# Optimization experiments

Measured on AMD Instinct MI355X. Metric: run time of the kernel, lower is better.

Reference implementation:

```python
import jax, jax.numpy as jnp
import numpy as np

C = 128          # channels
L = 2            # num_layers
NA = 30000       # nodes of type 'a'
NB = 30000       # nodes of type 'b'
E = 150000       # edges per edge type
SEED_SIZE = 1024
EPS = 1e-5


def _ln(x, g, b):
    # LayerNorm over last dim (biased variance, eps=1e-5), matches nn.LayerNorm / PyG LayerNorm(mode='node')
    m = x.mean(-1, keepdims=True)
    v = ((x - m) ** 2).mean(-1, keepdims=True)
    return (x - m) * jax.lax.rsqrt(v + EPS) * g + b


def _seg_mean(msg, dst, n):
    # PyG aggr='mean': mean of incoming messages, 0 for isolated nodes
    s = jax.ops.segment_sum(msg, dst, num_segments=n)
    cnt = jax.ops.segment_sum(jnp.ones((dst.shape[0],), msg.dtype), dst, num_segments=n)
    return s / jnp.maximum(cnt, 1.0)[:, None]


def _prmp_conv(x_src, x_dst, edge, w1, b1, w2, b2, g, be, uw, ub):
    src, dst = edge[0], edge[1]
    xi = x_dst[dst]                                   # [E, C] dst feats per edge
    xj = x_src[src]                                   # [E, C] src feats per edge
    h = jax.nn.relu(jax.lax.stop_gradient(xi) @ w1 + b1)  # pred_mlp on detached x_i
    pred = h @ w2 + b2
    msg = _ln(xj - pred, g, be)                       # LayerNorm(residual) per edge
    agg = _seg_mean(msg, dst, x_dst.shape[0])         # mean aggregation to dst nodes
    return jax.nn.relu(jnp.concatenate([x_dst, agg], -1) @ uw + ub)  # update_mlp


def setup_inputs() -> dict:
    key = jax.random.key(0)
    ks = jax.random.split(key, 12)
    edge_ab = jnp.stack([jax.random.randint(ks[2], (E,), 0, NA, jnp.int32),
                         jax.random.randint(ks[3], (E,), 0, NB, jnp.int32)])
    edge_ba = jnp.stack([jax.random.randint(ks[4], (E,), 0, NB, jnp.int32),
                         jax.random.randint(ks[5], (E,), 0, NA, jnp.int32)])
    return {
        "x_a": jax.random.normal(ks[0], (NA, C), jnp.float32),
        "x_b": jax.random.normal(ks[1], (NB, C), jnp.float32),
        "edge_ab": edge_ab,
        "edge_ba": edge_ba,
        "pred_w1": jax.random.normal(ks[6], (L, 2, C, C), jnp.float32) * 0.05,
        "pred_b1": jnp.zeros((L, 2, C), jnp.float32),
        "pred_w2": jax.random.normal(ks[7], (L, 2, C, C), jnp.float32) * 0.05,
        "pred_b2": jnp.zeros((L, 2, C), jnp.float32),
        "msg_gamma": jnp.ones((L, 2, C), jnp.float32),
        "msg_beta": jnp.zeros((L, 2, C), jnp.float32),
        "upd_w": jax.random.normal(ks[8], (L, 2, 2 * C, C), jnp.float32) * 0.05,
        "upd_b": jnp.zeros((L, 2, C), jnp.float32),
        "node_gamma": jnp.ones((L, 2, C), jnp.float32),
        "node_beta": jnp.zeros((L, 2, C), jnp.float32),
        "head_w": jax.random.normal(ks[9], (C, 1), jnp.float32) * 0.05,
        "head_b": jnp.zeros((1,), jnp.float32),
        "seed_size": SEED_SIZE,
    }


def reference(x_a, x_b, edge_ab, edge_ba, pred_w1, pred_b1, pred_w2, pred_b2,
              msg_gamma, msg_beta, upd_w, upd_b, node_gamma, node_beta,
              head_w, head_b, seed_size):
    enc = lambda t: jnp.nan_to_num(t, nan=0.0, posinf=1.0, neginf=-1.0)
    x_a, x_b = enc(x_a), enc(x_b)
    for l in range(L):
        # edge type 0: a -> b ; edge type 1: b -> a (HeteroConv aggr='sum' is trivial: one conv per dst type)
        nb = _prmp_conv(x_a, x_b, edge_ab, pred_w1[l, 0], pred_b1[l, 0], pred_w2[l, 0], pred_b2[l, 0],
                        msg_gamma[l, 0], msg_beta[l, 0], upd_w[l, 0], upd_b[l, 0])
        na = _prmp_conv(x_b, x_a, edge_ba, pred_w1[l, 1], pred_b1[l, 1], pred_w2[l, 1], pred_b2[l, 1],
                        msg_gamma[l, 1], msg_beta[l, 1], upd_w[l, 1], upd_b[l, 1])
        na = jnp.nan_to_num(na, nan=0.0, posinf=10.0, neginf=-10.0)
        nb = jnp.nan_to_num(nb, nan=0.0, posinf=10.0, neginf=-10.0)
        x_a = jax.nn.relu(_ln(na, node_gamma[l, 0], node_beta[l, 0]))
        x_b = jax.nn.relu(_ln(nb, node_gamma[l, 1], node_beta[l, 1]))
    # head: single Linear(C -> 1) on the seed nodes of the entity table (type 'a')
    return x_a[:seed_size] @ head_w + head_b
```

## Files before the change

kernel.cpp:

```cpp
#include <hip/hip_runtime.h>

#define CC 128
#define SCAN_T 1024
#define SCAN_I 4

typedef __attribute__((ext_vector_type(8))) short bf16x8;
typedef __attribute__((ext_vector_type(4))) float f32x4;
#define MFMA16(a, b, c) __builtin_amdgcn_mfma_f32_16x16x32_bf16(a, b, c, 0, 0, 0)

__device__ __forceinline__ float enc_nan(float v) {
    if (v != v) return 0.f;
    if (v > 3.0e38f) return 1.f;
    if (v < -3.0e38f) return -1.f;
    return v;
}

__device__ __forceinline__ ushort f2bf(float x) {
    unsigned u = __builtin_bit_cast(unsigned, x);
    u += 0x7fff + ((u >> 16) & 1);
    return (ushort)(u >> 16);
}
__device__ __forceinline__ float bf2f(ushort h) {
    return __builtin_bit_cast(float, ((unsigned)h) << 16);
}

__device__ __forceinline__ int swz128(int row, int k) { return (row * 128 + k) ^ ((row & 7) << 3); }

__global__ __launch_bounds__(256)
void k_setup(const float* __restrict__ xa_in, ushort* __restrict__ xa,
             float2* __restrict__ stat_a, int NA,
             const float* __restrict__ xb_in, ushort* __restrict__ xb,
             float2* __restrict__ stat_b, int NB,
             const float* __restrict__ pw1, const float* __restrict__ pw2,
             const float* __restrict__ uw,
             ushort* __restrict__ w1t, ushort* __restrict__ w2t, ushort* __restrict__ uwt,
             const int* __restrict__ dst_b, int Eab, int* __restrict__ cnt_b,
             const int* __restrict__ dst_a, int Eba, int* __restrict__ cnt_a,
             int Ginit, int Gwcvt)
{
    const int b = blockIdx.x;
    const int tid = threadIdx.x;
    if (b < Ginit) {
        int row = b * 8 + (tid >> 5);
        int s = tid & 31;
        const float* xin; ushort* xo; float2* st;
        if (row < NA) { xin = xa_in; xo = xa; st = stat_a; }
        else {
            row -= NA;
            if (row >= NB) return;
            xin = xb_in; xo = xb; st = stat_b;
        }
        float4 v = *reinterpret_cast<const float4*>(xin + (size_t)row * CC + s * 4);
        ushort h0 = f2bf(enc_nan(v.x)), h1 = f2bf(enc_nan(v.y));
        ushort h2 = f2bf(enc_nan(v.z)), h3 = f2bf(enc_nan(v.w));
        *reinterpret_cast<ushort4*>(xo + (size_t)row * CC + s * 4) = make_ushort4(h0, h1, h2, h3);
        float r0 = bf2f(h0), r1 = bf2f(h1), r2 = bf2f(h2), r3 = bf2f(h3);
        float sm = (r0 + r1) + (r2 + r3);
        float sq = fmaf(r0, r0, fmaf(r1, r1, fmaf(r2, r2, r3 * r3)));
        #pragma unroll
        for (int m = 1; m < 32; m <<= 1) { sm += __shfl_xor(sm, m); sq += __shfl_xor(sq, m); }
        if (s == 0) st[row] = make_float2(sm, sq);
    } else if (b < Ginit + Gwcvt) {
        int i = (b - Ginit) * 256 + tid;
        int t = i >> 16;
        int r = i & 65535;
        if (r < 16384) {
            int k = r >> 7, c = r & 127;
            w1t[(size_t)t * 16384 + c * 128 + k] = f2bf(pw1[(size_t)t * 16384 + k * 128 + c]);
        } else if (r < 32768) {
            int rr = r - 16384;
            int k = rr >> 7, c = rr & 127;
            w2t[(size_t)t * 16384 + c * 128 + k] = f2bf(pw2[(size_t)t * 16384 + k * 128 + c]);
        } else {
            int rr = r - 32768;
            int k = rr >> 7, c = rr & 127;
            uwt[(size_t)t * 32768 + c * 256 + k] = f2bf(uw[(size_t)t * 32768 + k * 128 + c]);
        }
    } else {
        int i = (b - Ginit - Gwcvt) * 256 + tid;
        if (i < Eab) atomicAdd(&cnt_b[dst_b[i]], 1);
        else if (i - Eab < Eba) atomicAdd(&cnt_a[dst_a[i - Eab]], 1);
    }
}

__global__ __launch_bounds__(SCAN_T)
void k_scan_dual(const int* __restrict__ cnt0, int* __restrict__ rowp0, int* __restrict__ off0, int n0,
                 const int* __restrict__ cnt1, int* __restrict__ rowp1, int* __restrict__ off1, int n1)
{
    const int* cnt = (blockIdx.x == 0) ? cnt0 : cnt1;
    int* row_ptr   = (blockIdx.x == 0) ? rowp0 : rowp1;
    int* off       = (blockIdx.x == 0) ? off0 : off1;
    int n          = (blockIdx.x == 0) ? n0 : n1;

    __shared__ int wsum[SCAN_T / 64];
    __shared__ int carry_s;
    const int tid = threadIdx.x, lane = tid & 63, wid = tid >> 6;
    if (tid == 0) carry_s = 0;
    __syncthreads();
    const int chunk = SCAN_T * SCAN_I;
    for (int base = 0; base < n; base += chunk) {
        int i0 = base + tid * SCAN_I;
        int v[SCAN_I];
        int local = 0;
        #pragma unroll
        for (int t = 0; t < SCAN_I; ++t) {
            int i = i0 + t;
            v[t] = (i < n) ? cnt[i] : 0;
            local += v[t];
        }
        int incl = local;
        #pragma unroll
        for (int d = 1; d < 64; d <<= 1) {
            int t = __shfl_up(incl, d);
            if (lane >= d) incl += t;
        }
        if (lane == 63) wsum[wid] = incl;
        __syncthreads();
        if (wid == 0) {
            int wv = (lane < SCAN_T / 64) ? wsum[lane] : 0;
            int winc = wv;
            #pragma unroll
            for (int d = 1; d < SCAN_T / 64; d <<= 1) {
                int t = __shfl_up(winc, d);
                if (lane >= d) winc += t;
            }
            if (lane < SCAN_T / 64) wsum[lane] = winc - wv;
        }
        __syncthreads();
        int carry = carry_s;
        int excl = carry + wsum[wid] + incl - local;
        #pragma unroll
        for (int t = 0; t < SCAN_I; ++t) {
            int i = i0 + t;
            if (i < n) { row_ptr[i] = excl; off[i] = excl; }
            excl += v[t];
        }
        __syncthreads();
        if (tid == SCAN_T - 1) carry_s = carry + wsum[SCAN_T / 64 - 1] + incl;
        __syncthreads();
    }
    if (threadIdx.x == 0) row_ptr[n] = carry_s;
}

__global__ __launch_bounds__(256)
void k_scatter_dual(const int* __restrict__ src_b, const int* __restrict__ dst_b, int Eab,
                    int* __restrict__ off_b, int* __restrict__ srcs_ab,
                    const int* __restrict__ src_a, const int* __restrict__ dst_a, int Eba,
                    int* __restrict__ off_a, int* __restrict__ srcs_ba)
{
    int i = blockIdx.x * 256 + threadIdx.x;
    if (i < Eab) {
        int p = atomicAdd(&off_b[dst_b[i]], 1);
        srcs_ab[p] = src_b[i];
    } else if (i - Eab < Eba) {
        int j = i - Eab;
        int p = atomicAdd(&off_a[dst_a[j]], 1);
        srcs_ba[p] = src_a[j];
    }
}

__device__ __forceinline__ void layer_body(
    char* smem,
    const ushort* __restrict__ xdst, const ushort* __restrict__ xsrc,
    const float2* __restrict__ stat_src,
    const int* __restrict__ rowp, const int* __restrict__ srcs,
    const ushort* __restrict__ w1t, const float* __restrict__ b1,
    const ushort* __restrict__ w2t, const float* __restrict__ b2,
    const float* __restrict__ mg, const float* __restrict__ mbt,
    const ushort* __restrict__ uwt, const float* __restrict__ ub,
    const float* __restrict__ ng, const float* __restrict__ nb,
    ushort* __restrict__ xout, float2* __restrict__ statOut, int N, int blk,
    const float* __restrict__ hw, const float* __restrict__ hb,
    float* __restrict__ hout, int headS)
{
    ushort* As = (ushort*)smem;
    ushort* Hs = (ushort*)(smem + 8192);
    ushort* P  = (ushort*)(smem + 16384);
    float (*os)[CC + 4] = (float(*)[CC + 4])(smem + 8192);

    const int tid = threadIdx.x;
    const int base = blk * 32;
    const int w = tid >> 6, l = tid & 63;
    const int lr = l & 15, lg = l >> 4;
    const int quarter = l >> 4;
    const int c8 = (l & 15) * 8;

    const int n0 = base + w * 8;
    int rp[9];
    #pragma unroll
    for (int i = 0; i < 9; ++i) {
        int nn = n0 + i;
        rp[i] = rowp[nn < N ? nn : N];
    }

    {
        int row = tid >> 3, k0 = (tid & 7) << 4;
        int node = base + row;
        bf16x8 v0 = {}, v1 = {};
        if (node < N) {
            v0 = *reinterpret_cast<const bf16x8*>(xdst + (size_t)node * CC + k0);
            v1 = *reinterpret_cast<const bf16x8*>(xdst + (size_t)node * CC + k0 + 8);
        }
        *reinterpret_cast<bf16x8*>(&As[swz128(row, k0)])     = v0;
        *reinterpret_cast<bf16x8*>(&As[swz128(row, k0 + 8)]) = v1;
    }
    __syncthreads();

    {
        f32x4 acc[2][2] = {};
        for (int kb = 0; kb < 4; ++kb) {
            int k = kb * 32 + lg * 8;
            bf16x8 a0 = *reinterpret_cast<const bf16x8*>(&As[swz128(lr, k)]);
            bf16x8 a1 = *reinterpret_cast<const bf16x8*>(&As[swz128(lr + 16, k)]);
            bf16x8 b0 = *reinterpret_cast<const bf16x8*>(&w1t[(size_t)(w * 32 + lr) * 128 + k]);
            bf16x8 b1v = *reinterpret_cast<const bf16x8*>(&w1t[(size_t)(w * 32 + 16 + lr) * 128 + k]);
            acc[0][0] = MFMA16(a0, b0, acc[0][0]);
            acc[0][1] = MFMA16(a0, b1v, acc[0][1]);
            acc[1][0] = MFMA16(a1, b0, acc[1][0]);
            acc[1][1] = MFMA16(a1, b1v, acc[1][1]);
        }
        float bc[2] = { b1[w * 32 + lr], b1[w * 32 + 16 + lr] };
        #pragma unroll
        for (int mi = 0; mi < 2; ++mi)
            #pragma unroll
            for (int ni = 0; ni < 2; ++ni) {
                int col = w * 32 + ni * 16 + lr;
                #pragma unroll
                for (int j = 0; j < 4; ++j) {
                    int row = mi * 16 + lg * 4 + j;
                    Hs[swz128(row, col)] = f2bf(fmaxf(acc[mi][ni][j] + bc[ni], 0.f));
                }
            }
    }
    __syncthreads();

    {
        f32x4 acc[2][2] = {};
        for (int kb = 0; kb < 4; ++kb) {
            int k = kb * 32 + lg * 8;
            bf16x8 a0 = *reinterpret_cast<const bf16x8*>(&Hs[swz128(lr, k)]);
            bf16x8 a1 = *reinterpret_cast<const bf16x8*>(&Hs[swz128(lr + 16, k)]);
            bf16x8 b0 = *reinterpret_cast<const bf16x8*>(&w2t[(size_t)(w * 32 + lr) * 128 + k]);
            bf16x8 b1v = *reinterpret_cast<const bf16x8*>(&w2t[(size_t)(w * 32 + 16 + lr) * 128 + k]);
            acc[0][0] = MFMA16(a0, b0, acc[0][0]);
            acc[0][1] = MFMA16(a0, b1v, acc[0][1]);
            acc[1][0] = MFMA16(a1, b0, acc[1][0]);
            acc[1][1] = MFMA16(a1, b1v, acc[1][1]);
        }
        float bc[2] = { b2[w * 32 + lr], b2[w * 32 + 16 + lr] };
        #pragma unroll
        for (int mi = 0; mi < 2; ++mi)
            #pragma unroll
            for (int ni = 0; ni < 2; ++ni) {
                int col = w * 32 + ni * 16 + lr;
                #pragma unroll
                for (int j = 0; j < 4; ++j) {
                    int row = mi * 16 + lg * 4 + j;
                    P[row * CC + col] = f2bf(acc[mi][ni][j] + bc[ni]);
                }
            }
    }
    __syncthreads();

    {
        const float4 g0 = *reinterpret_cast<const float4*>(mg + c8);
        const float4 g1 = *reinterpret_cast<const float4*>(mg + c8 + 4);
        const float4 e0 = *reinterpret_cast<const float4*>(mbt + c8);
        const float4 e1 = *reinterpret_cast<const float4*>(mbt + c8 + 4);
        const float gv[8] = { g0.x, g0.y, g0.z, g0.w, g1.x, g1.y, g1.z, g1.w };
        const float bv[8] = { e0.x, e0.y, e0.z, e0.w, e1.x, e1.y, e1.z, e1.w };

        int pj = rp[0] + quarter;
        bool phave = pj < rp[1];
        int psidx = srcs[phave ? pj : 0];
        bf16x8 pxv = *reinterpret_cast<const bf16x8*>(xsrc + (size_t)psidx * CC + c8);
        float2 pst = stat_src[psidx];

        for (int i = 0; i < 8; ++i) {
            const int nl_ = w * 8 + i;
            const int d = n0 + i;
            bool chave = phave;
            bf16x8 cxv = pxv;
            float2 cst = pst;
            int cj = rp[i] + quarter;
            const int je = rp[i + 1];
            if (i < 7) {
                pj = rp[i + 1] + quarter;
                phave = pj < rp[i + 2];
                psidx = srcs[phave ? pj : 0];
                pxv = *reinterpret_cast<const bf16x8*>(xsrc + (size_t)psidx * CC + c8);
                pst = stat_src[psidx];
            }
            if (d >= N) continue;

            bf16x8 prb = *reinterpret_cast<const bf16x8*>(&P[nl_ * CC + c8]);
            float pr[8];
            #pragma unroll
            for (int q = 0; q < 8; ++q) pr[q] = bf2f((ushort)prb[q]);
            float sp = 0.f, qp = 0.f;
            #pragma unroll
            for (int q = 0; q < 8; ++q) { sp += pr[q]; qp = fmaf(pr[q], pr[q], qp); }
            #pragma unroll
            for (int m = 1; m < 16; m <<= 1) { sp += __shfl_xor(sp, m); qp += __shfl_xor(qp, m); }
            const int deg = je - rp[i];
            float a[8] = {};
            float rsum = 0.f, cmsum = 0.f;

            while (chave) {
                int jn = cj + 4;
                bool nhave = jn < je;
                bf16x8 nxv = cxv; float2 nst = cst;
                if (nhave) {
                    int nsidx = srcs[jn];
                    nxv = *reinterpret_cast<const bf16x8*>(xsrc + (size_t)nsidx * CC + c8);
                    nst = stat_src[nsidx];
                }
                float xj[8];
                #pragma unroll
                for (int q = 0; q < 8; ++q) xj[q] = bf2f((ushort)cxv[q]);
                float dot = 0.f;
                #pragma unroll
                for (int q = 0; q < 8; ++q) dot = fmaf(xj[q], pr[q], dot);
                #pragma unroll
                for (int m = 1; m < 16; m <<= 1) dot += __shfl_xor(dot, m);
                const float mean = (cst.x - sp) * (1.f / 128.f);
                const float var = fmaf(-2.f, dot, cst.y + qp) * (1.f / 128.f) - mean * mean;
                const float r = rsqrtf(var + 1e-5f);
                rsum += r;
                cmsum = fmaf(mean, r, cmsum);
                #pragma unroll
                for (int q = 0; q < 8; ++q) a[q] = fmaf(xj[q], r, a[q]);
                cj = jn; chave = nhave; cxv = nxv; cst = nst;
            }
            #pragma unroll
            for (int q = 0; q < 8; ++q) { a[q] += __shfl_xor(a[q], 16); a[q] += __shfl_xor(a[q], 32); }
            rsum += __shfl_xor(rsum, 16);  rsum += __shfl_xor(rsum, 32);
            cmsum += __shfl_xor(cmsum, 16); cmsum += __shfl_xor(cmsum, 32);
            if (quarter == 0) {
                ushort o8[8];
                if (deg > 0) {
                    const float inv = 1.f / (float)deg;
                    #pragma unroll
                    for (int q = 0; q < 8; ++q)
                        o8[q] = f2bf(fmaf((a[q] - pr[q] * rsum - cmsum) * inv, gv[q], bv[q]));
                } else {
                    #pragma unroll
                    for (int q = 0; q < 8; ++q) o8[q] = 0;
                }
                *reinterpret_cast<bf16x8*>(&Hs[swz128(nl_, c8)]) = *reinterpret_cast<bf16x8*>(&o8[0]);
            }
        }
    }
    __syncthreads();

    f32x4 acc[2][2] = {};
    for (int kb = 0; kb < 8; ++kb) {
        int k = kb * 32 + lg * 8;
        const ushort* Ab = (k < 128) ? As : Hs;
        int kl = k & 127;
        bf16x8 a0 = *reinterpret_cast<const bf16x8*>(&Ab[swz128(lr, kl)]);
        bf16x8 a1 = *reinterpret_cast<const bf16x8*>(&Ab[swz128(lr + 16, kl)]);
        bf16x8 b0 = *reinterpret_cast<const bf16x8*>(&uwt[(size_t)(w * 32 + lr) * 256 + k]);
        bf16x8 b1v = *reinterpret_cast<const bf16x8*>(&uwt[(size_t)(w * 32 + 16 + lr) * 256 + k]);
        acc[0][0] = MFMA16(a0, b0, acc[0][0]);
        acc[0][1] = MFMA16(a0, b1v, acc[0][1]);
        acc[1][0] = MFMA16(a1, b0, acc[1][0]);
        acc[1][1] = MFMA16(a1, b1v, acc[1][1]);
    }
    __syncthreads();

    {
        float bc[2] = { ub[w * 32 + lr], ub[w * 32 + 16 + lr] };
        #pragma unroll
        for (int mi = 0; mi < 2; ++mi)
            #pragma unroll
            for (int ni = 0; ni < 2; ++ni) {
                int col = w * 32 + ni * 16 + lr;
                #pragma unroll
                for (int j = 0; j < 4; ++j) {
                    int row = mi * 16 + lg * 4 + j;
                    os[row][col] = fmaxf(acc[mi][ni][j] + bc[ni], 0.f);
                }
            }
    }
    __syncthreads();

    const int nl = w * 8 + (l >> 3);
    const int cl = l & 7;
    float vals[16];
    float sm = 0.f, sq = 0.f;
    #pragma unroll
    for (int t = 0; t < 16; ++t) {
        float u = os[nl][cl + 8 * t];
        vals[t] = u; sm += u; sq = fmaf(u, u, sq);
    }
    #pragma unroll
    for (int m = 1; m < 8; m <<= 1) { sm += __shfl_xor(sm, m); sq += __shfl_xor(sq, m); }
    float mean = sm * (1.f / 128.f);
    float var = sq * (1.f / 128.f) - mean * mean;
    float r = rsqrtf(var + 1e-5f);
    int node = base + nl;
    if (node < N) {
        float so = 0.f, sqo = 0.f, hsum = 0.f;
        bool doHead = (node < headS);
        #pragma unroll
        for (int t = 0; t < 16; ++t) {
            int cch = cl + 8 * t;
            float o = fmaxf(fmaf((vals[t] - mean) * r, ng[cch], nb[cch]), 0.f);
            ushort ob = f2bf(o);
            xout[(size_t)node * CC + cch] = ob;
            float orr = bf2f(ob);
            so += orr; sqo = fmaf(orr, orr, sqo);
            if (doHead) hsum = fmaf(o, hw[cch], hsum);
        }
        #pragma unroll
        for (int m = 1; m < 8; m <<= 1) { so += __shfl_xor(so, m); sqo += __shfl_xor(sqo, m); }
        if (doHead) {
            #pragma unroll
            for (int m = 1; m < 8; m <<= 1) hsum += __shfl_xor(hsum, m);
            if (cl == 0) hout[node] = hsum + hb[0];
        }
        if (cl == 0) statOut[node] = make_float2(so, sqo);
    }
}

__global__ __launch_bounds__(256)
void k_layer_dual(
    const ushort* __restrict__ xb_c, const ushort* __restrict__ xa_c,
    const float2* __restrict__ stat_a_c, const float2* __restrict__ stat_b_c,
    const int* __restrict__ rowp_b, const int* __restrict__ srcs_ab,
    const int* __restrict__ rowp_a, const int* __restrict__ srcs_ba,
    ushort* __restrict__ xb_n, ushort* __restrict__ xa_n,
    float2* __restrict__ stat_b_n, float2* __restrict__ stat_a_n,
    int NB, int NA, int GB,
    const ushort* __restrict__ w1t0, const float* __restrict__ b10,
    const ushort* __restrict__ w2t0, const float* __restrict__ b20,
    const float* __restrict__ mg0, const float* __restrict__ mb0,
    const ushort* __restrict__ uwt0, const float* __restrict__ ub0,
    const float* __restrict__ ng0, const float* __restrict__ nb0,
    const ushort* __restrict__ w1t1, const float* __restrict__ b11,
    const ushort* __restrict__ w2t1, const float* __restrict__ b21,
    const float* __restrict__ mg1, const float* __restrict__ mb1,
    const ushort* __restrict__ uwt1, const float* __restrict__ ub1,
    const float* __restrict__ ng1, const float* __restrict__ nb1,
    const float* __restrict__ hw, const float* __restrict__ hb,
    float* __restrict__ hout, int headS)
{
    __shared__ __align__(16) char smem[25088];
    if ((int)blockIdx.x < GB)
        layer_body(smem, xb_c, xa_c, stat_a_c, rowp_b, srcs_ab,
                   w1t0, b10, w2t0, b20, mg0, mb0, uwt0, ub0, ng0, nb0,
                   xb_n, stat_b_n, NB, blockIdx.x, hw, hb, hout, 0);
    else
        layer_body(smem, xa_c, xb_c, stat_b_c, rowp_a, srcs_ba,
                   w1t1, b11, w2t1, b21, mg1, mb1, uwt1, ub1, ng1, nb1,
                   xa_n, stat_a_n, NA, blockIdx.x - GB, hw, hb, hout, headS);
}

extern "C" void kernel_launch(void* const* d_in, const int* in_sizes, int n_in,
                              void* d_out, int out_size, void* d_ws, size_t ws_size,
                              hipStream_t stream)
{
    const float* x_a_in = (const float*)d_in[0];
    const float* x_b_in = (const float*)d_in[1];
    const int*   e_ab   = (const int*)d_in[2];
    const int*   e_ba   = (const int*)d_in[3];
    const float* pw1    = (const float*)d_in[4];
    const float* pb1    = (const float*)d_in[5];
    const float* pw2    = (const float*)d_in[6];
    const float* pb2    = (const float*)d_in[7];
    const float* mgam   = (const float*)d_in[8];
    const float* mbet   = (const float*)d_in[9];
    const float* uw     = (const float*)d_in[10];
    const float* ubias  = (const float*)d_in[11];
    const float* ngam   = (const float*)d_in[12];
    const float* nbet   = (const float*)d_in[13];
    const float* hw     = (const float*)d_in[14];
    const float* hb     = (const float*)d_in[15];

    const int NA  = in_sizes[0] / CC;
    const int NB  = in_sizes[1] / CC;
    const int Eab = in_sizes[2] / 2;
    const int Eba = in_sizes[3] / 2;

    float* ws = (float*)d_ws;
    size_t off = 0;
    ushort* xa0 = (ushort*)(ws + off); off += (size_t)NA * CC / 2;
    ushort* xa1 = (ushort*)(ws + off); off += (size_t)NA * CC / 2;
    ushort* xb0 = (ushort*)(ws + off); off += (size_t)NB * CC / 2;
    ushort* xb1 = (ushort*)(ws + off); off += (size_t)NB * CC / 2;
    float2* sa0 = (float2*)(ws + off); off += (size_t)NA * 2;
    float2* sa1 = (float2*)(ws + off); off += (size_t)NA * 2;
    float2* sb0 = (float2*)(ws + off); off += (size_t)NB * 2;
    float2* sb1 = (float2*)(ws + off); off += (size_t)NB * 2;
    ushort* w1t = (ushort*)(ws + off); off += 4 * 16384 / 2;
    ushort* w2t = (ushort*)(ws + off); off += 4 * 16384 / 2;
    ushort* uwt = (ushort*)(ws + off); off += 4 * 32768 / 2;
    int* iw = (int*)(ws + off);
    size_t ioff = 0;
    int* cnt_b   = iw + ioff; ioff += NB;
    int* cnt_a   = iw + ioff; ioff += NA;
    int* rowp_b  = iw + ioff; ioff += NB + 1;
    int* rowp_a  = iw + ioff; ioff += NA + 1;
    int* off_b   = iw + ioff; ioff += NB;
    int* off_a   = iw + ioff; ioff += NA;
    int* srcs_ab = iw + ioff; ioff += Eab;
    int* srcs_ba = iw + ioff; ioff += Eba;

    const int GB = (NB + 31) / 32, GA = (NA + 31) / 32;
    const int Ginit = (NA + NB + 7) / 8;
    const int Gwcvt = 1024;
    const int Ghist = (Eab + Eba + 255) / 256;

    hipMemsetAsync(cnt_b, 0, (size_t)(NB + NA) * sizeof(int), stream);
    k_setup<<<dim3(Ginit + Gwcvt + Ghist), dim3(256), 0, stream>>>(
        x_a_in, xa0, sa0, NA, x_b_in, xb0, sb0, NB,
        pw1, pw2, uw, w1t, w2t, uwt,
        e_ab + Eab, Eab, cnt_b, e_ba + Eba, Eba, cnt_a,
        Ginit, Gwcvt);
    k_scan_dual<<<dim3(2), dim3(SCAN_T), 0, stream>>>(
        cnt_b, rowp_b, off_b, NB, cnt_a, rowp_a, off_a, NA);
    k_scatter_dual<<<dim3((Eab + Eba + 255) / 256), dim3(256), 0, stream>>>(
        e_ab, e_ab + Eab, Eab, off_b, srcs_ab,
        e_ba, e_ba + Eba, Eba, off_a, srcs_ba);

    ushort* xac = xa0; ushort* xan = xa1;
    ushort* xbc = xb0; ushort* xbn = xb1;
    float2* sac = sa0; float2* san = sa1;
    float2* sbc = sb0; float2* sbn = sb1;

    for (int lyr = 0; lyr < 2; ++lyr) {
        int t0 = lyr * 2 + 0;
        int t1 = lyr * 2 + 1;
        int headS = (lyr == 1) ? out_size : 0;

        k_layer_dual<<<dim3(GB + GA), dim3(256), 0, stream>>>(
            xbc, xac, sac, sbc,
            rowp_b, srcs_ab, rowp_a, srcs_ba,
            xbn, xan, sbn, san,
            NB, NA, GB,
            w1t + (size_t)t0 * 16384, pb1 + t0 * CC, w2t + (size_t)t0 * 16384, pb2 + t0 * CC,
            mgam + t0 * CC, mbet + t0 * CC,
            uwt + (size_t)t0 * 32768, ubias + t0 * CC, ngam + t0 * CC, nbet + t0 * CC,
            w1t + (size_t)t1 * 16384, pb1 + t1 * CC, w2t + (size_t)t1 * 16384, pb2 + t1 * CC,
            mgam + t1 * CC, mbet + t1 * CC,
            uwt + (size_t)t1 * 32768, ubias + t1 * CC, ngam + t1 * CC, nbet + t1 * CC,
            hw, hb, (float*)d_out, headS);

        ushort* t;
        t = xac; xac = xan; xan = t;
        t = xbc; xbc = xbn; xbn = t;
        float2* s;
        s = sac; sac = san; san = s;
        s = sbc; sbc = sbn; sbn = s;
    }
}
```

Baseline: 242.4 us.

## Halve nodes per block to 16 and drop software-pipelined edge gather

Each block now handles 16 destination nodes instead of 32, doubling the grid and halving shared memory per block, with the MFMA tiles reduced to a single 16-row M tile. The edge-gather loop loses its prefetch-next-edge software pipelining and the per-warp row-pointer preload, reading rowp directly per node. The aim is more blocks in flight for better occupancy and load balance over the irregular gathers. The cost is that each weight tile loaded from global memory feeds half as many MFMAs, and gather latency is no longer hidden inside each thread.

```diff
diff --git a/kernel.cpp b/kernel.cpp
--- a/kernel.cpp
+++ b/kernel.cpp
@@ -174,91 +174,70 @@
     float* __restrict__ hout, int headS)
 {
     ushort* As = (ushort*)smem;
-    ushort* Hs = (ushort*)(smem + 8192);
-    ushort* P  = (ushort*)(smem + 16384);
-    float (*os)[CC + 4] = (float(*)[CC + 4])(smem + 8192);
+    ushort* Hs = (ushort*)(smem + 4096);
+    ushort* P  = (ushort*)(smem + 8192);
+    float (*os)[CC + 4] = (float(*)[CC + 4])smem;
 
     const int tid = threadIdx.x;
-    const int base = blk * 32;
+    const int base = blk * 16;
     const int w = tid >> 6, l = tid & 63;
     const int lr = l & 15, lg = l >> 4;
     const int quarter = l >> 4;
     const int c8 = (l & 15) * 8;
 
-    const int n0 = base + w * 8;
-    int rp[9];
-    #pragma unroll
-    for (int i = 0; i < 9; ++i) {
-        int nn = n0 + i;
-        rp[i] = rowp[nn < N ? nn : N];
-    }
-
     {
-        int row = tid >> 3, k0 = (tid & 7) << 4;
+        int row = tid >> 4, k0 = (tid & 15) << 3;
         int node = base + row;
-        bf16x8 v0 = {}, v1 = {};
-        if (node < N) {
+        bf16x8 v0 = {};
+        if (node < N)
             v0 = *reinterpret_cast<const bf16x8*>(xdst + (size_t)node * CC + k0);
-            v1 = *reinterpret_cast<const bf16x8*>(xdst + (size_t)node * CC + k0 + 8);
-        }
-        *reinterpret_cast<bf16x8*>(&As[swz128(row, k0)])     = v0;
-        *reinterpret_cast<bf16x8*>(&As[swz128(row, k0 + 8)]) = v1;
+        *reinterpret_cast<bf16x8*>(&As[swz128(row, k0)]) = v0;
     }
     __syncthreads();
 
     {
-        f32x4 acc[2][2] = {};
+        f32x4 acc[2] = {};
         for (int kb = 0; kb < 4; ++kb) {
             int k = kb * 32 + lg * 8;
             bf16x8 a0 = *reinterpret_cast<const bf16x8*>(&As[swz128(lr, k)]);
-            bf16x8 a1 = *reinterpret_cast<const bf16x8*>(&As[swz128(lr + 16, k)]);
             bf16x8 b0 = *reinterpret_cast<const bf16x8*>(&w1t[(size_t)(w * 32 + lr) * 128 + k]);
             bf16x8 b1v = *reinterpret_cast<const bf16x8*>(&w1t[(size_t)(w * 32 + 16 + lr) * 128 + k]);
-            acc[0][0] = MFMA16(a0, b0, acc[0][0]);
-            acc[0][1] = MFMA16(a0, b1v, acc[0][1]);
-            acc[1][0] = MFMA16(a1, b0, acc[1][0]);
-            acc[1][1] = MFMA16(a1, b1v, acc[1][1]);
+            acc[0] = MFMA16(a0, b0, acc[0]);
+            acc[1] = MFMA16(a0, b1v, acc[1]);
         }
         float bc[2] = { b1[w * 32 + lr], b1[w * 32 + 16 + lr] };
         #pragma unroll
-        for (int mi = 0; mi < 2; ++mi)
-            #pragma unroll
-            for (int ni = 0; ni < 2; ++ni) {
-                int col = w * 32 + ni * 16 + lr;
-                #pragma unroll
-                for (int j = 0; j < 4; ++j) {
-                    int row = mi * 16 + lg * 4 + j;
-                    Hs[swz128(row, col)] = f2bf(fmaxf(acc[mi][ni][j] + bc[ni], 0.f));
-                }
+        for (int ni = 0; ni < 2; ++ni) {
+            int col = w * 32 + ni * 16 + lr;
+            #pragma unroll
+            for (int j = 0; j < 4; ++j) {
+                int row = lg * 4 + j;
+                Hs[swz128(row, col)] = f2bf(fmaxf(acc[ni][j] + bc[ni], 0.f));
             }
+        }
     }
     __syncthreads();
 
     {
-        f32x4 acc[2][2] = {};
+        f32x4 acc[2] = {};
         for (int kb = 0; kb < 4; ++kb) {
             int k = kb * 32 + lg * 8;
             bf16x8 a0 = *reinterpret_cast<const bf16x8*>(&Hs[swz128(lr, k)]);
-            bf16x8 a1 = *reinterpret_cast<const bf16x8*>(&Hs[swz128(lr + 16, k)]);
             bf16x8 b0 = *reinterpret_cast<const bf16x8*>(&w2t[(size_t)(w * 32 + lr) * 128 + k]);
             bf16x8 b1v = *reinterpret_cast<const bf16x8*>(&w2t[(size_t)(w * 32 + 16 + lr) * 128 + k]);
-            acc[0][0] = MFMA16(a0, b0, acc[0][0]);
-            acc[0][1] = MFMA16(a0, b1v, acc[0][1]);
-            acc[1][0] = MFMA16(a1, b0, acc[1][0]);
-            acc[1][1] = MFMA16(a1, b1v, acc[1][1]);
+            acc[0] = MFMA16(a0, b0, acc[0]);
+            acc[1] = MFMA16(a0, b1v, acc[1]);
         }
         float bc[2] = { b2[w * 32 + lr], b2[w * 32 + 16 + lr] };
         #pragma unroll
-        for (int mi = 0; mi < 2; ++mi)
-            #pragma unroll
-            for (int ni = 0; ni < 2; ++ni) {
-                int col = w * 32 + ni * 16 + lr;
-                #pragma unroll
-                for (int j = 0; j < 4; ++j) {
-                    int row = mi * 16 + lg * 4 + j;
-                    P[row * CC + col] = f2bf(acc[mi][ni][j] + bc[ni]);
-                }
+        for (int ni = 0; ni < 2; ++ni) {
+            int col = w * 32 + ni * 16 + lr;
+            #pragma unroll
+            for (int j = 0; j < 4; ++j) {
+                int row = lg * 4 + j;
+                P[row * CC + col] = f2bf(acc[ni][j] + bc[ni]);
             }
+        }
     }
     __syncthreads();
 
@@ -269,30 +248,10 @@
         const float4 e1 = *reinterpret_cast<const float4*>(mbt + c8 + 4);
         const float gv[8] = { g0.x, g0.y, g0.z, g0.w, g1.x, g1.y, g1.z, g1.w };
         const float bv[8] = { e0.x, e0.y, e0.z, e0.w, e1.x, e1.y, e1.z, e1.w };
-
-        int pj = rp[0] + quarter;
-        bool phave = pj < rp[1];
-        int psidx = srcs[phave ? pj : 0];
-        bf16x8 pxv = *reinterpret_cast<const bf16x8*>(xsrc + (size_t)psidx * CC + c8);
-        float2 pst = stat_src[psidx];
-
-        for (int i = 0; i < 8; ++i) {
-            const int nl_ = w * 8 + i;
-            const int d = n0 + i;
-            bool chave = phave;
-            bf16x8 cxv = pxv;
-            float2 cst = pst;
-            int cj = rp[i] + quarter;
-            const int je = rp[i + 1];
-            if (i < 7) {
-                pj = rp[i + 1] + quarter;
-                phave = pj < rp[i + 2];
-                psidx = srcs[phave ? pj : 0];
-                pxv = *reinterpret_cast<const bf16x8*>(xsrc + (size_t)psidx * CC + c8);
-                pst = stat_src[psidx];
-            }
-            if (d >= N) continue;
-
+        for (int i = 0; i < 4; ++i) {
+            const int nl_ = w * 4 + i;
+            const int d = base + nl_;
+            if (d >= N) break;
             bf16x8 prb = *reinterpret_cast<const bf16x8*>(&P[nl_ * CC + c8]);
             float pr[8];
             #pragma unroll
@@ -302,35 +261,29 @@
             for (int q = 0; q < 8; ++q) { sp += pr[q]; qp = fmaf(pr[q], pr[q], qp); }
             #pragma unroll
             for (int m = 1; m < 16; m <<= 1) { sp += __shfl_xor(sp, m); qp += __shfl_xor(qp, m); }
-            const int deg = je - rp[i];
+            const int jb = rowp[d], je = rowp[d + 1];
+            const int deg = je - jb;
             float a[8] = {};
             float rsum = 0.f, cmsum = 0.f;
-
-            while (chave) {
-                int jn = cj + 4;
-                bool nhave = jn < je;
-                bf16x8 nxv = cxv; float2 nst = cst;
-                if (nhave) {
-                    int nsidx = srcs[jn];
-                    nxv = *reinterpret_cast<const bf16x8*>(xsrc + (size_t)nsidx * CC + c8);
-                    nst = stat_src[nsidx];
-                }
+            for (int j = jb + quarter; j < je; j += 4) {
+                const int sidx = srcs[j];
+                bf16x8 xb_ = *reinterpret_cast<const bf16x8*>(xsrc + (size_t)sidx * CC + c8);
+                const float2 st = stat_src[sidx];
                 float xj[8];
                 #pragma unroll
-                for (int q = 0; q < 8; ++q) xj[q] = bf2f((ushort)cxv[q]);
+                for (int q = 0; q < 8; ++q) xj[q] = bf2f((ushort)xb_[q]);
                 float dot = 0.f;
                 #pragma unroll
                 for (int q = 0; q < 8; ++q) dot = fmaf(xj[q], pr[q], dot);
                 #pragma unroll
                 for (int m = 1; m < 16; m <<= 1) dot += __shfl_xor(dot, m);
-                const float mean = (cst.x - sp) * (1.f / 128.f);
-                const float var = fmaf(-2.f, dot, cst.y + qp) * (1.f / 128.f) - mean * mean;
+                const float mean = (st.x - sp) * (1.f / 128.f);
+                const float var = fmaf(-2.f, dot, st.y + qp) * (1.f / 128.f) - mean * mean;
                 const float r = rsqrtf(var + 1e-5f);
                 rsum += r;
                 cmsum = fmaf(mean, r, cmsum);
                 #pragma unroll
                 for (int q = 0; q < 8; ++q) a[q] = fmaf(xj[q], r, a[q]);
-                cj = jn; chave = nhave; cxv = nxv; cst = nst;
             }
             #pragma unroll
             for (int q = 0; q < 8; ++q) { a[q] += __shfl_xor(a[q], 16); a[q] += __shfl_xor(a[q], 32); }
@@ -353,49 +306,44 @@
     }
     __syncthreads();
 
-    f32x4 acc[2][2] = {};
+    f32x4 acc[2] = {};
     for (int kb = 0; kb < 8; ++kb) {
         int k = kb * 32 + lg * 8;
         const ushort* Ab = (k < 128) ? As : Hs;
         int kl = k & 127;
         bf16x8 a0 = *reinterpret_cast<const bf16x8*>(&Ab[swz128(lr, kl)]);
-        bf16x8 a1 = *reinterpret_cast<const bf16x8*>(&Ab[swz128(lr + 16, kl)]);
         bf16x8 b0 = *reinterpret_cast<const bf16x8*>(&uwt[(size_t)(w * 32 + lr) * 256 + k]);
         bf16x8 b1v = *reinterpret_cast<const bf16x8*>(&uwt[(size_t)(w * 32 + 16 + lr) * 256 + k]);
-        acc[0][0] = MFMA16(a0, b0, acc[0][0]);
-        acc[0][1] = MFMA16(a0, b1v, acc[0][1]);
-        acc[1][0] = MFMA16(a1, b0, acc[1][0]);
-        acc[1][1] = MFMA16(a1, b1v, acc[1][1]);
+        acc[0] = MFMA16(a0, b0, acc[0]);
+        acc[1] = MFMA16(a0, b1v, acc[1]);
     }
     __syncthreads();
 
     {
         float bc[2] = { ub[w * 32 + lr], ub[w * 32 + 16 + lr] };
         #pragma unroll
-        for (int mi = 0; mi < 2; ++mi)
-            #pragma unroll
-            for (int ni = 0; ni < 2; ++ni) {
-                int col = w * 32 + ni * 16 + lr;
-                #pragma unroll
-                for (int j = 0; j < 4; ++j) {
-                    int row = mi * 16 + lg * 4 + j;
-                    os[row][col] = fmaxf(acc[mi][ni][j] + bc[ni], 0.f);
-                }
+        for (int ni = 0; ni < 2; ++ni) {
+            int col = w * 32 + ni * 16 + lr;
+            #pragma unroll
+            for (int j = 0; j < 4; ++j) {
+                int row = lg * 4 + j;
+                os[row][col] = fmaxf(acc[ni][j] + bc[ni], 0.f);
             }
-    }
-    __syncthreads();
-
-    const int nl = w * 8 + (l >> 3);
-    const int cl = l & 7;
-    float vals[16];
+        }
+    }
+    __syncthreads();
+
+    const int nl = w * 4 + (l >> 4);
+    const int cl = l & 15;
+    float vals[8];
     float sm = 0.f, sq = 0.f;
     #pragma unroll
-    for (int t = 0; t < 16; ++t) {
-        float u = os[nl][cl + 8 * t];
+    for (int t = 0; t < 8; ++t) {
+        float u = os[nl][cl + 16 * t];
         vals[t] = u; sm += u; sq = fmaf(u, u, sq);
     }
     #pragma unroll
-    for (int m = 1; m < 8; m <<= 1) { sm += __shfl_xor(sm, m); sq += __shfl_xor(sq, m); }
+    for (int m = 1; m < 16; m <<= 1) { sm += __shfl_xor(sm, m); sq += __shfl_xor(sq, m); }
     float mean = sm * (1.f / 128.f);
     float var = sq * (1.f / 128.f) - mean * mean;
     float r = rsqrtf(var + 1e-5f);
@@ -404,8 +352,8 @@
         float so = 0.f, sqo = 0.f, hsum = 0.f;
         bool doHead = (node < headS);
         #pragma unroll
-        for (int t = 0; t < 16; ++t) {
-            int cch = cl + 8 * t;
+        for (int t = 0; t < 8; ++t) {
+            int cch = cl + 16 * t;
             float o = fmaxf(fmaf((vals[t] - mean) * r, ng[cch], nb[cch]), 0.f);
             ushort ob = f2bf(o);
             xout[(size_t)node * CC + cch] = ob;
@@ -414,10 +362,10 @@
             if (doHead) hsum = fmaf(o, hw[cch], hsum);
         }
         #pragma unroll
-        for (int m = 1; m < 8; m <<= 1) { so += __shfl_xor(so, m); sqo += __shfl_xor(sqo, m); }
+        for (int m = 1; m < 16; m <<= 1) { so += __shfl_xor(so, m); sqo += __shfl_xor(sqo, m); }
         if (doHead) {
             #pragma unroll
-            for (int m = 1; m < 8; m <<= 1) hsum += __shfl_xor(hsum, m);
+            for (int m = 1; m < 16; m <<= 1) hsum += __shfl_xor(hsum, m);
             if (cl == 0) hout[node] = hsum + hb[0];
         }
         if (cl == 0) statOut[node] = make_float2(so, sqo);
@@ -446,7 +394,7 @@
     const float* __restrict__ hw, const float* __restrict__ hb,
     float* __restrict__ hout, int headS)
 {
-    __shared__ __align__(16) char smem[25088];
+    __shared__ __align__(16) char smem[12288];
     if ((int)blockIdx.x < GB)
         layer_body(smem, xb_c, xa_c, stat_a_c, rowp_b, srcs_ab,
                    w1t0, b10, w2t0, b20, mg0, mb0, uwt0, ub0, ng0, nb0,
@@ -507,7 +455,7 @@
     int* srcs_ab = iw + ioff; ioff += Eab;
     int* srcs_ba = iw + ioff; ioff += Eba;
 
-    const int GB = (NB + 31) / 32, GA = (NA + 31) / 32;
+    const int GB = (NB + 15) / 16, GA = (NA + 15) / 16;
     const int Ginit = (NA + NB + 7) / 8;
     const int Gwcvt = 1024;
     const int Ghist = (Eab + Eba + 255) / 256;
```

Result: slower. 271.5 us (+12.0%).
